# Performance work log

Measured on AMD Instinct MI355X. Metric: run time of the kernel, lower is better.

The kernel has to match this reference:

```python
import jax, jax.numpy as jnp
import numpy as np

D = 512      # model dim
NH = 8       # heads
DH = 64      # dim per head
M = 256      # num landmarks
ITERS = 6    # pinv iterations
EPS = 1e-5   # layernorm eps


def layer_norm(x, g, b):
    mu = x.mean(-1, keepdims=True)
    var = ((x - mu) ** 2).mean(-1, keepdims=True)
    return (x - mu) * jax.lax.rsqrt(var + EPS) * g + b


def moore_penrose_pinv(x, iters=ITERS):
    abs_x = jnp.abs(x)
    col = abs_x.sum(-1)
    row = abs_x.sum(-2)
    z = jnp.swapaxes(x, -1, -2) / (jnp.max(col) * jnp.max(row))
    I = jnp.eye(x.shape[-1], dtype=x.dtype)
    for _ in range(iters):
        xz = x @ z
        z = 0.25 * z @ (13 * I - xz @ (15 * I - xz @ (7 * I - xz)))
    return z


def nystrom_attention(x, w_qkv, w_out, b_out, res_w):
    B, n0, _ = x.shape
    pad = (M - n0 % M) % M
    x = jnp.pad(x, ((0, 0), (pad, 0), (0, 0)))  # pad at front, like lucidrains
    n = n0 + pad
    qkv = x @ w_qkv  # (B, n, 3*D), no bias
    q, k, v = jnp.split(qkv, 3, axis=-1)
    rs = lambda t: t.reshape(B, n, NH, DH).transpose(0, 2, 1, 3)  # (B,H,n,d)
    q = rs(q) * (DH ** -0.5)
    k = rs(k)
    v = rs(v)
    l = n // M
    q_l = q.reshape(B, NH, M, l, DH).mean(3)  # (B,H,M,d) landmark means
    k_l = k.reshape(B, NH, M, l, DH).mean(3)
    s1 = jnp.einsum('bhnd,bhmd->bhnm', q, k_l)
    s2 = jnp.einsum('bhmd,bhld->bhml', q_l, k_l)
    s3 = jnp.einsum('bhmd,bhnd->bhmn', q_l, k)
    a1 = jax.nn.softmax(s1, -1)
    a2 = jax.nn.softmax(s2, -1)
    a3 = jax.nn.softmax(s3, -1)
    out = a1 @ (moore_penrose_pinv(a2) @ (a3 @ v))  # (B,H,n,d)
    # depthwise residual conv over sequence: Conv2d(heads, heads, (33,1), groups=heads)
    res = jax.lax.conv_general_dilated(v, res_w, (1, 1), 'SAME',
                                       feature_group_count=NH,
                                       dimension_numbers=('NCHW', 'OIHW', 'NCHW'))
    out = out + res
    out = out.transpose(0, 2, 1, 3).reshape(B, n, NH * DH) @ w_out + b_out
    return out[:, -n0:]


def dwconv(x, w, b):
    y = jax.lax.conv_general_dilated(x, w, (1, 1), 'SAME',
                                     feature_group_count=x.shape[1],
                                     dimension_numbers=('NCHW', 'OIHW', 'NCHW'))
    return y + b[None, :, None, None]


def ppeg(x, pw7, pb7, pw5, pb5, pw3, pb3, Hh, Ww):
    cls, feat = x[:, :1], x[:, 1:]
    B, _, C = x.shape
    cnn = feat.transpose(0, 2, 1).reshape(B, C, Hh, Ww)
    y = cnn + dwconv(cnn, pw7, pb7) + dwconv(cnn, pw5, pb5) + dwconv(cnn, pw3, pb3)
    y = y.reshape(B, C, Hh * Ww).transpose(0, 2, 1)
    return jnp.concatenate([cls, y], axis=1)


def _forward(x, w_fc1, b_fc1, cls_token, ln1_g, ln1_b, qkv1_w, out1_w, out1_b, res1_w,
             ln2_g, ln2_b, qkv2_w, out2_w, out2_b, res2_w,
             pw7, pb7, pw5, pb5, pw3, pb3, lnf_g, lnf_b, w_fc2, b_fc2):
    h = jax.nn.relu(x @ w_fc1 + b_fc1)  # (B, N, 512)
    Hn = h.shape[1]
    s = int(np.ceil(np.sqrt(Hn)))  # static grid side
    add = s * s - Hn
    h = jnp.concatenate([h, h[:, :add]], axis=1)
    B = h.shape[0]
    cls = jnp.broadcast_to(cls_token, (B, 1, D))
    h = jnp.concatenate([cls, h], axis=1)
    h = h + nystrom_attention(layer_norm(h, ln1_g, ln1_b), qkv1_w, out1_w, out1_b, res1_w)
    h = ppeg(h, pw7, pb7, pw5, pb5, pw3, pb3, s, s)
    h = h + nystrom_attention(layer_norm(h, ln2_g, ln2_b), qkv2_w, out2_w, out2_b, res2_w)
    h = layer_norm(h, lnf_g, lnf_b)[:, 0]
    return h @ w_fc2 + b_fc2


def setup_inputs() -> dict:
    key = jax.random.key(0)
    ks = jax.random.split(key, 16)
    g = lambda k, shp, s=0.02: jax.random.normal(k, shp, dtype=jnp.float32) * s
    z = lambda n: jnp.zeros((n,), jnp.float32)
    o = lambda n: jnp.ones((n,), jnp.float32)
    B, N, DIN, NC = 2, 10000, 1024, 2
    return {
        'x': jax.random.normal(ks[0], (B, N, DIN), dtype=jnp.float32),
        'w_fc1': g(ks[1], (DIN, D)), 'b_fc1': z(D),
        'cls_token': g(ks[2], (1, 1, D), 1.0),
        'ln1_g': o(D), 'ln1_b': z(D),
        'qkv1_w': g(ks[3], (D, 3 * D)),
        'out1_w': g(ks[4], (D, D)), 'out1_b': z(D),
        'res1_w': g(ks[5], (NH, 1, 33, 1)),
        'ln2_g': o(D), 'ln2_b': z(D),
        'qkv2_w': g(ks[6], (D, 3 * D)),
        'out2_w': g(ks[7], (D, D)), 'out2_b': z(D),
        'res2_w': g(ks[8], (NH, 1, 33, 1)),
        'pw7': g(ks[9], (D, 1, 7, 7)), 'pb7': z(D),
        'pw5': g(ks[10], (D, 1, 5, 5)), 'pb5': z(D),
        'pw3': g(ks[11], (D, 1, 3, 3)), 'pb3': z(D),
        'lnf_g': o(D), 'lnf_b': z(D),
        'w_fc2': g(ks[12], (D, NC)), 'b_fc2': z(NC),
    }


def reference(x, w_fc1, b_fc1, cls_token, ln1_g, ln1_b, qkv1_w, out1_w, out1_b, res1_w,
              ln2_g, ln2_b, qkv2_w, out2_w, out2_b, res2_w,
              pw7, pb7, pw5, pb5, pw3, pb3, lnf_g, lnf_b, w_fc2, b_fc2):
    logits = _forward(x, w_fc1, b_fc1, cls_token, ln1_g, ln1_b, qkv1_w, out1_w, out1_b, res1_w,
                      ln2_g, ln2_b, qkv2_w, out2_w, out2_b, res2_w,
                      pw7, pb7, pw5, pb5, pw3, pb3, lnf_g, lnf_b, w_fc2, b_fc2)
    Y_prob = jax.nn.softmax(logits, -1)
    Y_hat = jnp.argmax(logits, -1)
    return logits, Y_prob, Y_hat
```

## Files before the change

kernel.cpp:

```cpp
#include <hip/hip_runtime.h>
#include <math.h>

#define FLAG_RELU 1
#define FLAG_BIAS 2
#define FLAG_ACC  4
#define FLAG_ATOMIC 8

static constexpr int BB   = 2;
static constexpr int N0   = 10000;
static constexpr int DIN  = 1024;
static constexpr int D    = 512;
static constexpr int NH   = 8;
static constexpr int DH   = 64;
static constexpr int MM   = 256;
static constexpr int SEQ  = 10240;
static constexpr int PADR = 239;
static constexpr int NTOK = 10001;
static constexpr int LL   = 40;
static constexpr float EPS_ = 1e-5f;

typedef short short8v __attribute__((ext_vector_type(8)));
typedef float f32x4 __attribute__((ext_vector_type(4)));

__device__ __forceinline__ void atomicMaxPosF(float* addr, float v) {
    atomicMax((unsigned int*)addr, __float_as_uint(v));
}
__device__ __forceinline__ ushort f2bf(float f) {
    unsigned u = __float_as_uint(f);
    return (ushort)((u + 0x7FFFu + ((u >> 16) & 1u)) >> 16);
}
__device__ __forceinline__ float bf2f(ushort h) {
    return __uint_as_float(((unsigned)h) << 16);
}
__device__ __forceinline__ void split4(float4 f, ushort* ph, ushort* pl) {
    ushort4 hv, lv;
    hv.x = f2bf(f.x); lv.x = f2bf(f.x - bf2f(hv.x));
    hv.y = f2bf(f.y); lv.y = f2bf(f.y - bf2f(hv.y));
    hv.z = f2bf(f.z); lv.z = f2bf(f.z - bf2f(hv.z));
    hv.w = f2bf(f.w); lv.w = f2bf(f.w - bf2f(hv.w));
    *(ushort4*)ph = hv; *(ushort4*)pl = lv;
}
__device__ __forceinline__ void split8r(const float* p, short8v& h, short8v& l) {
    ushort hb[8], lb[8];
    split4(*(const float4*)p,     &hb[0], &lb[0]);
    split4(*(const float4*)(p+4), &hb[4], &lb[4]);
    h = *(short8v*)hb; l = *(short8v*)lb;
}

__global__ __launch_bounds__(256)
void mgemm128(const float* __restrict__ A, int lda, long long sAz,
              const ushort* __restrict__ BtH, const ushort* __restrict__ BtL, int ldbt,
              float* __restrict__ C, int ldc, long long sCz, const float* __restrict__ bias,
              int M, int N, int K, int flags, int qcols, float qscale)
{
    __shared__ ushort AsH[4*128*8], AsL[4*128*8], BsH[4*128*8], BsL[4*128*8];
    A += (size_t)blockIdx.z * sAz;
    C += (size_t)blockIdx.z * sCz;
    int t = threadIdx.x;
    int m0 = blockIdx.y * 128, n0 = blockIdx.x * 128;
    int w = t >> 6, lane = t & 63, q = lane >> 4, r = lane & 15;
    int wm = w >> 1, wn = w & 1;
    f32x4 acc[4][4];
    #pragma unroll
    for (int i = 0; i < 4; i++)
        #pragma unroll
        for (int j = 0; j < 4; j++) acc[i][j] = (f32x4){0.f,0.f,0.f,0.f};

    int srow = t >> 1, scg = (t & 1) * 16;
    int qg = (t & 1) * 2;
    int gm = m0 + srow;
    float4 pa0, pa1, pa2, pa3;
    uint4  pb0, pb1, pb2, pb3;
    {
        pa0 = pa1 = pa2 = pa3 = make_float4(0,0,0,0);
        if (gm < M) {
            const float* ap = A + (size_t)gm * lda + scg;
            pa0 = *(const float4*)(ap);   pa1 = *(const float4*)(ap+4);
            pa2 = *(const float4*)(ap+8); pa3 = *(const float4*)(ap+12);
        }
        size_t gb = (size_t)(n0 + srow) * ldbt + scg;
        pb0 = *(const uint4*)(BtH + gb); pb1 = *(const uint4*)(BtH + gb + 8);
        pb2 = *(const uint4*)(BtL + gb); pb3 = *(const uint4*)(BtL + gb + 8);
    }
    for (int k0 = 0; k0 < K; k0 += 32) {
        {
            ushort hb[16], lb[16];
            split4(pa0, &hb[0],  &lb[0]);
            split4(pa1, &hb[4],  &lb[4]);
            split4(pa2, &hb[8],  &lb[8]);
            split4(pa3, &hb[12], &lb[12]);
            *(uint4*)&AsH[(qg  )*1024 + srow*8] = *(uint4*)&hb[0];
            *(uint4*)&AsH[(qg+1)*1024 + srow*8] = *(uint4*)&hb[8];
            *(uint4*)&AsL[(qg  )*1024 + srow*8] = *(uint4*)&lb[0];
            *(uint4*)&AsL[(qg+1)*1024 + srow*8] = *(uint4*)&lb[8];
            *(uint4*)&BsH[(qg  )*1024 + srow*8] = pb0;
            *(uint4*)&BsH[(qg+1)*1024 + srow*8] = pb1;
            *(uint4*)&BsL[(qg  )*1024 + srow*8] = pb2;
            *(uint4*)&BsL[(qg+1)*1024 + srow*8] = pb3;
        }
        __syncthreads();
        if (k0 + 32 < K) {
            pa0 = pa1 = pa2 = pa3 = make_float4(0,0,0,0);
            if (gm < M) {
                const float* ap = A + (size_t)gm * lda + k0 + 32 + scg;
                pa0 = *(const float4*)(ap);   pa1 = *(const float4*)(ap+4);
                pa2 = *(const float4*)(ap+8); pa3 = *(const float4*)(ap+12);
            }
            size_t gb = (size_t)(n0 + srow) * ldbt + k0 + 32 + scg;
            pb0 = *(const uint4*)(BtH + gb); pb1 = *(const uint4*)(BtH + gb + 8);
            pb2 = *(const uint4*)(BtL + gb); pb3 = *(const uint4*)(BtL + gb + 8);
        }
        short8v ah[4], al[4];
        #pragma unroll
        for (int mi = 0; mi < 4; mi++) {
            int row = wm*64 + mi*16 + r;
            ah[mi] = *(const short8v*)&AsH[q*1024 + row*8];
            al[mi] = *(const short8v*)&AsL[q*1024 + row*8];
        }
        #pragma unroll
        for (int ni = 0; ni < 4; ni++) {
            int col = wn*64 + ni*16 + r;
            short8v bh = *(const short8v*)&BsH[q*1024 + col*8];
            short8v bl = *(const short8v*)&BsL[q*1024 + col*8];
            #pragma unroll
            for (int mi = 0; mi < 4; mi++) {
                acc[mi][ni] = __builtin_amdgcn_mfma_f32_16x16x32_bf16(ah[mi], bh, acc[mi][ni], 0,0,0);
                acc[mi][ni] = __builtin_amdgcn_mfma_f32_16x16x32_bf16(ah[mi], bl, acc[mi][ni], 0,0,0);
                acc[mi][ni] = __builtin_amdgcn_mfma_f32_16x16x32_bf16(al[mi], bh, acc[mi][ni], 0,0,0);
            }
        }
        __syncthreads();
    }
    #pragma unroll
    for (int mi = 0; mi < 4; mi++)
        #pragma unroll
        for (int ni = 0; ni < 4; ni++) {
            int gcol = n0 + wn*64 + ni*16 + r;
            float qs = (gcol < qcols) ? qscale : 1.f;
            float bv = (flags & FLAG_BIAS) ? bias[gcol] : 0.f;
            #pragma unroll
            for (int rg = 0; rg < 4; rg++) {
                int grow = m0 + wm*64 + mi*16 + q*4 + rg;
                if (grow >= M) continue;
                float v = acc[mi][ni][rg] * qs + bv;
                if (flags & FLAG_RELU) v = fmaxf(v, 0.f);
                float* cp = C + (size_t)grow * ldc + gcol;
                if (flags & FLAG_ACC) v += *cp;
                *cp = v;
            }
        }
}

__global__ __launch_bounds__(256)
void mbgemm64(const float* __restrict__ Abase, long long sAb, long long sAh, long long sAz, int lda,
              const ushort* __restrict__ BtH, const ushort* __restrict__ BtL,
              const float* __restrict__ Bnt, long long sBb, long long sBh, int ldb,
              float* __restrict__ Cbase, long long sCb, long long sCh, long long sCz, int ldc,
              ushort* __restrict__ eTH, ushort* __restrict__ eTL, long long sT, int ldct,
              const float* __restrict__ rowM, const float* __restrict__ rowI,
              int M, int N, int K, int nchunk,
              float dg, float bsc, float osc, int slab0, int flags)
{
    __shared__ ushort AsH[4*64*8], AsL[4*64*8], BsH[4*64*8], BsL[4*64*8];
    int zi = blockIdx.z / nchunk, ch = blockIdx.z % nchunk;
    int g = slab0 + zi, b = g >> 3, h = g & 7;
    const float* A = Abase + (size_t)b*sAb + (size_t)h*sAh + (size_t)zi*sAz;
    float* C = Cbase ? (Cbase + (size_t)b*sCb + (size_t)h*sCh + (size_t)zi*sCz) : nullptr;
    int kpc = K / nchunk;
    int kb = ch * kpc, ke = kb + kpc;
    int t = threadIdx.x;
    int m0 = blockIdx.y * 64, n0 = blockIdx.x * 64;
    int w = t >> 6, lane = t & 63, q = lane >> 4, r = lane & 15;
    int wm = w >> 1, wn = w & 1;
    f32x4 acc[2][2];
    #pragma unroll
    for (int i = 0; i < 2; i++)
        #pragma unroll
        for (int j = 0; j < 2; j++) acc[i][j] = (f32x4){0.f,0.f,0.f,0.f};

    int srow = t >> 2, scg = (t & 3) * 8;
    int qg = t & 3;
    float rmv = 0.f, riv = 1.f;
    bool doexp = (rowM != nullptr);
    if (doexp) {
        rmv = rowM[(size_t)zi * MM + m0 + srow];
        riv = rowI[(size_t)zi * MM + m0 + srow];
    }
    const float* Abp = Bnt ? (Bnt + (size_t)b*sBb + (size_t)h*sBh) : nullptr;
    float4 pa0, pa1;
    float4 pf0, pf1;
    uint4  pu0, pu1;
    {
        const float* ap = A + (size_t)(m0 + srow) * lda + kb + scg;
        pa0 = *(const float4*)ap; pa1 = *(const float4*)(ap+4);
        if (Bnt) {
            const float* bp = Abp + (size_t)(n0 + srow) * ldb + kb + scg;
            pf0 = *(const float4*)bp; pf1 = *(const float4*)(bp+4);
        } else {
            size_t gb = (size_t)b*sBb + (size_t)h*sBh + (size_t)(n0 + srow) * ldb + kb + scg;
            pu0 = *(const uint4*)(BtH + gb); pu1 = *(const uint4*)(BtL + gb);
        }
    }
    for (int k0 = kb; k0 < ke; k0 += 32) {
        {
            float4 qa0 = pa0, qa1 = pa1;
            if (doexp) {
                qa0.x = expf(qa0.x - rmv) * riv; qa0.y = expf(qa0.y - rmv) * riv;
                qa0.z = expf(qa0.z - rmv) * riv; qa0.w = expf(qa0.w - rmv) * riv;
                qa1.x = expf(qa1.x - rmv) * riv; qa1.y = expf(qa1.y - rmv) * riv;
                qa1.z = expf(qa1.z - rmv) * riv; qa1.w = expf(qa1.w - rmv) * riv;
            }
            ushort hb[8], lb[8];
            split4(qa0, &hb[0], &lb[0]);
            split4(qa1, &hb[4], &lb[4]);
            *(uint4*)&AsH[qg*512 + srow*8] = *(uint4*)&hb[0];
            *(uint4*)&AsL[qg*512 + srow*8] = *(uint4*)&lb[0];
            if (Bnt) {
                ushort hc[8], lc[8];
                split4(pf0, &hc[0], &lc[0]);
                split4(pf1, &hc[4], &lc[4]);
                *(uint4*)&BsH[qg*512 + srow*8] = *(uint4*)&hc[0];
                *(uint4*)&BsL[qg*512 + srow*8] = *(uint4*)&lc[0];
            } else {
                *(uint4*)&BsH[qg*512 + srow*8] = pu0;
                *(uint4*)&BsL[qg*512 + srow*8] = pu1;
            }
        }
        __syncthreads();
        if (k0 + 32 < ke) {
            const float* ap = A + (size_t)(m0 + srow) * lda + k0 + 32 + scg;
            pa0 = *(const float4*)ap; pa1 = *(const float4*)(ap+4);
            if (Bnt) {
                const float* bp = Abp + (size_t)(n0 + srow) * ldb + k0 + 32 + scg;
                pf0 = *(const float4*)bp; pf1 = *(const float4*)(bp+4);
            } else {
                size_t gb = (size_t)b*sBb + (size_t)h*sBh + (size_t)(n0 + srow) * ldb + k0 + 32 + scg;
                pu0 = *(const uint4*)(BtH + gb); pu1 = *(const uint4*)(BtL + gb);
            }
        }
        short8v ah[2], al[2];
        #pragma unroll
        for (int mi = 0; mi < 2; mi++) {
            int row = wm*32 + mi*16 + r;
            ah[mi] = *(const short8v*)&AsH[q*512 + row*8];
            al[mi] = *(const short8v*)&AsL[q*512 + row*8];
        }
        #pragma unroll
        for (int ni = 0; ni < 2; ni++) {
            int col = wn*32 + ni*16 + r;
            short8v bh = *(const short8v*)&BsH[q*512 + col*8];
            short8v bl = *(const short8v*)&BsL[q*512 + col*8];
            #pragma unroll
            for (int mi = 0; mi < 2; mi++) {
                acc[mi][ni] = __builtin_amdgcn_mfma_f32_16x16x32_bf16(ah[mi], bh, acc[mi][ni], 0,0,0);
                acc[mi][ni] = __builtin_amdgcn_mfma_f32_16x16x32_bf16(ah[mi], bl, acc[mi][ni], 0,0,0);
                acc[mi][ni] = __builtin_amdgcn_mfma_f32_16x16x32_bf16(al[mi], bh, acc[mi][ni], 0,0,0);
            }
        }
        __syncthreads();
    }
    bool dgnz = (dg != 0.f);
    #pragma unroll
    for (int mi = 0; mi < 2; mi++)
        #pragma unroll
        for (int ni = 0; ni < 2; ni++) {
            int gm0 = m0 + wm*32 + mi*16 + q*4;
            int gn  = n0 + wn*32 + ni*16 + r;
            float v[4];
            #pragma unroll
            for (int rg = 0; rg < 4; rg++) {
                float u = bsc * acc[mi][ni][rg];
                if (dgnz) u += dg * A[(size_t)(gm0+rg) * lda + gn];
                v[rg] = osc * u;
            }
            if (C) {
                if (flags & FLAG_ATOMIC) {
                    #pragma unroll
                    for (int rg = 0; rg < 4; rg++)
                        atomicAdd(C + (size_t)(gm0+rg) * ldc + gn, v[rg]);
                } else {
                    #pragma unroll
                    for (int rg = 0; rg < 4; rg++)
                        C[(size_t)(gm0+rg) * ldc + gn] = v[rg];
                }
            }
            if (eTH) {
                ushort4 hv, lv;
                hv.x = f2bf(v[0]); lv.x = f2bf(v[0] - bf2f(hv.x));
                hv.y = f2bf(v[1]); lv.y = f2bf(v[1] - bf2f(hv.y));
                hv.z = f2bf(v[2]); lv.z = f2bf(v[2] - bf2f(hv.z));
                hv.w = f2bf(v[3]); lv.w = f2bf(v[3] - bf2f(hv.w));
                size_t to = (size_t)g * sT + (size_t)gn * ldct + gm0;
                *(ushort4*)(eTH + to) = hv;
                *(ushort4*)(eTL + to) = lv;
            }
        }
}

__global__ __launch_bounds__(256)
void a1_fused(const float* __restrict__ qkv,
              const ushort* __restrict__ klH, const ushort* __restrict__ klL,
              const ushort* __restrict__ wbH, const ushort* __restrict__ wbL,
              float* __restrict__ attn)
{
    constexpr int LP = 264;
    __shared__ ushort PcH[32*LP], PcL[32*LP];
    __shared__ float redm[4][32];
    __shared__ float reds[4][32];
    int g = blockIdx.y, b = g >> 3, h = g & 7;
    int tok0 = blockIdx.x * 32;
    int t = threadIdx.x;
    int w = t >> 6, lane = t & 63, q = lane >> 4, r = lane & 15;

    f32x4 acc[2][4];
    #pragma unroll
    for (int i = 0; i < 2; i++)
        #pragma unroll
        for (int j = 0; j < 4; j++) acc[i][j] = (f32x4){0.f,0.f,0.f,0.f};
    #pragma unroll
    for (int k0 = 0; k0 < 64; k0 += 32) {
        short8v ah[2], al[2];
        #pragma unroll
        for (int mi = 0; mi < 2; mi++) {
            const float* ap = qkv + ((size_t)b*SEQ + tok0 + mi*16 + r) * 1536
                            + h*DH + k0 + q*8;
            split8r(ap, ah[mi], al[mi]);
        }
        #pragma unroll
        for (int ni = 0; ni < 4; ni++) {
            size_t kb = ((size_t)g*MM + w*64 + ni*16 + r) * DH + k0 + q*8;
            short8v bh = *(const short8v*)(klH + kb);
            short8v bl = *(const short8v*)(klL + kb);
            #pragma unroll
            for (int mi = 0; mi < 2; mi++) {
                acc[mi][ni] = __builtin_amdgcn_mfma_f32_16x16x32_bf16(ah[mi], bh, acc[mi][ni], 0,0,0);
                acc[mi][ni] = __builtin_amdgcn_mfma_f32_16x16x32_bf16(ah[mi], bl, acc[mi][ni], 0,0,0);
                acc[mi][ni] = __builtin_amdgcn_mfma_f32_16x16x32_bf16(al[mi], bh, acc[mi][ni], 0,0,0);
            }
        }
    }
    #pragma unroll
    for (int mi = 0; mi < 2; mi++)
        #pragma unroll
        for (int rg = 0; rg < 4; rg++) {
            float m = fmaxf(fmaxf(acc[mi][0][rg], acc[mi][1][rg]),
                            fmaxf(acc[mi][2][rg], acc[mi][3][rg]));
            for (int o = 8; o > 0; o >>= 1) m = fmaxf(m, __shfl_xor(m, o));
            if (r == 0) redm[w][mi*16 + q*4 + rg] = m;
        }
    __syncthreads();
    #pragma unroll
    for (int mi = 0; mi < 2; mi++)
        #pragma unroll
        for (int rg = 0; rg < 4; rg++) {
            int row = mi*16 + q*4 + rg;
            float gm = fmaxf(fmaxf(redm[0][row], redm[1][row]),
                             fmaxf(redm[2][row], redm[3][row]));
            float s = 0.f;
            #pragma unroll
            for (int ni = 0; ni < 4; ni++) {
                float e = expf(acc[mi][ni][rg] - gm);
                acc[mi][ni][rg] = e;
                s += e;
                int col = w*64 + ni*16 + r;
                ushort hv = f2bf(e);
                PcH[row*LP + col] = hv;
                PcL[row*LP + col] = f2bf(e - bf2f(hv));
            }
            for (int o = 8; o > 0; o >>= 1) s += __shfl_xor(s, o);
            if (r == 0) reds[w][row] = s;
        }
    __syncthreads();
    int wm = w & 1, wn = w >> 1;
    int prow = wm*16 + r;
    f32x4 oacc[2];
    #pragma unroll
    for (int ni = 0; ni < 2; ni++) oacc[ni] = (f32x4){0.f,0.f,0.f,0.f};
    #pragma unroll
    for (int k0 = 0; k0 < 8; k0++) {
        short8v ph = *(const short8v*)&PcH[prow*LP + k0*32 + q*8];
        short8v pl = *(const short8v*)&PcL[prow*LP + k0*32 + q*8];
        #pragma unroll
        for (int ni = 0; ni < 2; ni++) {
            size_t wo = ((size_t)g*64 + wn*32 + ni*16 + r) * MM + k0*32 + q*8;
            short8v bh = *(const short8v*)(wbH + wo);
            short8v bl = *(const short8v*)(wbL + wo);
            oacc[ni] = __builtin_amdgcn_mfma_f32_16x16x32_bf16(ph, bh, oacc[ni], 0,0,0);
            oacc[ni] = __builtin_amdgcn_mfma_f32_16x16x32_bf16(ph, bl, oacc[ni], 0,0,0);
            oacc[ni] = __builtin_amdgcn_mfma_f32_16x16x32_bf16(pl, bh, oacc[ni], 0,0,0);
        }
    }
    float inv[4];
    #pragma unroll
    for (int rg = 0; rg < 4; rg++) {
        int row = wm*16 + q*4 + rg;
        inv[rg] = 1.0f / (reds[0][row] + reds[1][row] + reds[2][row] + reds[3][row]);
    }
    #pragma unroll
    for (int ni = 0; ni < 2; ni++)
        #pragma unroll
        for (int rg = 0; rg < 4; rg++) {
            int tok = tok0 + wm*16 + q*4 + rg;
            attn[((size_t)b*SEQ + tok) * D + h*DH + wn*32 + ni*16 + r] = oacc[ni][rg] * inv[rg];
        }
}

__global__ __launch_bounds__(256)
void convsplitT(const float* __restrict__ in, ushort* __restrict__ oh, ushort* __restrict__ ol,
                int R, int C, int ldin, long long sInB, long long sInH, long long sInZ,
                int ldo, long long sOutZ)
{
    __shared__ float tile[32][33];
    int z = blockIdx.z, b = z >> 3, h = z & 7;
    const float* I = in + (size_t)b*sInB + (size_t)h*sInH + (size_t)z*sInZ;
    int p0 = blockIdx.x * 32, c0 = blockIdx.y * 32;
    int tx = threadIdx.x & 31, ty = threadIdx.x >> 5;
    #pragma unroll
    for (int k = 0; k < 4; k++) {
        int rr = p0 + ty + k*8, cc = c0 + tx;
        tile[ty + k*8][tx] = (rr < R && cc < C) ? I[(size_t)rr * ldin + cc] : 0.f;
    }
    __syncthreads();
    #pragma unroll
    for (int k = 0; k < 4; k++) {
        int rr = p0 + tx, cc = c0 + ty + k*8;
        if (rr < R && cc < C) {
            float f = tile[tx][ty + k*8];
            ushort hv = f2bf(f);
            size_t o = (size_t)z * sOutZ + (size_t)cc * ldo + rr;
            oh[o] = hv; ol[o] = f2bf(f - bf2f(hv));
        }
    }
}

__global__ void fill_cls(const float* __restrict__ cls, float* __restrict__ H) {
    H[(size_t)blockIdx.x * NTOK * D + threadIdx.x] = cls[threadIdx.x];
}

__global__ __launch_bounds__(256)
void ln_pad(const float* __restrict__ H, const float* __restrict__ g,
            const float* __restrict__ bt, float* __restrict__ out)
{
    int blk = blockIdx.x;
    int b = blk / SEQ, i = blk % SEQ;
    int t = threadIdx.x;
    float* orow = out + (size_t)blk * D;
    if (i < PADR) { orow[t] = 0.f; orow[t+256] = 0.f; return; }
    const float* x = H + ((size_t)b * NTOK + (i - PADR)) * D;
    float v0 = x[t], v1 = x[t+256];
    __shared__ float w1[4], w2[4];
    float s = v0 + v1;
    for (int o = 32; o > 0; o >>= 1) s += __shfl_xor(s, o);
    if ((t & 63) == 0) w1[t >> 6] = s;
    __syncthreads();
    float mu = (w1[0]+w1[1]+w1[2]+w1[3]) * (1.0f / D);
    float d0 = v0 - mu, d1 = v1 - mu;
    float qq = d0*d0 + d1*d1;
    for (int o = 32; o > 0; o >>= 1) qq += __shfl_xor(qq, o);
    if ((t & 63) == 0) w2[t >> 6] = qq;
    __syncthreads();
    float rs = rsqrtf((w2[0]+w2[1]+w2[2]+w2[3]) * (1.0f / D) + EPS_);
    orow[t]     = d0 * rs * g[t]     + bt[t];
    orow[t+256] = d1 * rs * g[t+256] + bt[t+256];
}

__global__ __launch_bounds__(512)
void landmarks(const float* __restrict__ qkv, float* __restrict__ ql,
               float* __restrict__ klt, ushort* __restrict__ klH, ushort* __restrict__ klL)
{
    int blk = blockIdx.x;
    int b = blk >> 8, m = blk & 255;
    int c = threadIdx.x;
    const float* base = qkv + ((size_t)b * SEQ + (size_t)m * LL) * 1536;
    float sq0=0,sq1=0,sq2=0,sq3=0, sk0=0,sk1=0,sk2=0,sk3=0;
    for (int tt = 0; tt < LL; tt += 4) {
        const float* rr = base + (size_t)tt * 1536;
        sq0 += rr[c];          sk0 += rr[512 + c];
        sq1 += rr[1536 + c];   sk1 += rr[1536 + 512 + c];
        sq2 += rr[3072 + c];   sk2 += rr[3072 + 512 + c];
        sq3 += rr[4608 + c];   sk3 += rr[4608 + 512 + c];
    }
    float sq = (sq0+sq1+sq2+sq3) * (1.0f / LL);
    float sk = (sk0+sk1+sk2+sk3) * (1.0f / LL);
    int h = c >> 6, d = c & 63;
    int slab = b * NH + h;
    ql [((size_t)slab * MM + m) * DH + d] = sq;
    klt[((size_t)slab * DH + d) * MM + m] = sk;
    size_t kidx = ((size_t)slab * MM + m) * DH + d;
    ushort kh = f2bf(sk);
    klH[kidx] = kh; klL[kidx] = f2bf(sk - bf2f(kh));
}

__global__ __launch_bounds__(256)
void s2_softmax(const float* __restrict__ ql, const float* __restrict__ klt,
                float* __restrict__ a2)
{
    int blk = blockIdx.x;
    int m = blk & 255, slab = blk >> 8;
    int j = threadIdx.x;
    __shared__ float q[64];
    __shared__ float red[256];
    if (j < 64) q[j] = ql[((size_t)slab * MM + m) * DH + j];
    __syncthreads();
    const float* kt = klt + (size_t)slab * DH * MM;
    float s = 0.f;
    #pragma unroll 8
    for (int kk = 0; kk < 64; kk++) s = fmaf(q[kk], kt[kk*MM + j], s);
    red[j] = s; __syncthreads();
    for (int o = 128; o > 0; o >>= 1) { if (j < o) red[j] = fmaxf(red[j], red[j+o]); __syncthreads(); }
    float mx = red[0]; __syncthreads();
    float e = expf(s - mx);
    red[j] = e; __syncthreads();
    for (int o = 128; o > 0; o >>= 1) { if (j < o) red[j] += red[j+o]; __syncthreads(); }
    a2[((size_t)slab * MM + m) * MM + j] = e / red[0];
}

__global__ void zero_scr(float* s) { if (threadIdx.x < 2) s[threadIdx.x] = 0.f; }

__global__ __launch_bounds__(256)
void a2_alpha(const float* __restrict__ a2, float* __restrict__ scr)
{
    int slab = blockIdx.x, t = threadIdx.x;
    const float* A = a2 + (size_t)slab * MM * MM;
    float cs = 0.f, rs = 0.f;
    for (int rr = 0; rr < MM; rr++) cs += fabsf(A[(size_t)rr * MM + t]);
    for (int cc = 0; cc < MM; cc++) rs += fabsf(A[(size_t)t * MM + cc]);
    __shared__ float red[256];
    red[t] = rs; __syncthreads();
    for (int o = 128; o > 0; o >>= 1) { if (t < o) red[t] = fmaxf(red[t], red[t+o]); __syncthreads(); }
    float mrs = red[0]; __syncthreads();
    red[t] = cs; __syncthreads();
    for (int o = 128; o > 0; o >>= 1) { if (t < o) red[t] = fmaxf(red[t], red[t+o]); __syncthreads(); }
    float mcs = red[0];
    if (t == 0) { atomicMaxPosF(scr + 0, mrs); atomicMaxPosF(scr + 1, mcs); }
}

__global__ __launch_bounds__(256)
void z_init(const float* __restrict__ a2, const float* __restrict__ scr,
            float* __restrict__ z, ushort* __restrict__ zTh, ushort* __restrict__ zTl)
{
    size_t idx = (size_t)blockIdx.x * 256 + threadIdx.x;
    int slab = (int)(idx >> 16), rr = (int)((idx >> 8) & 255), cc = (int)(idx & 255);
    float inv = 1.0f / (scr[0] * scr[1]);
    z[idx] = a2[((size_t)slab << 16) + (size_t)cc * MM + rr] * inv;
    float tv = a2[idx] * inv;
    ushort th = f2bf(tv);
    zTh[idx] = th; zTl[idx] = f2bf(tv - bf2f(th));
}

__global__ __launch_bounds__(256)
void s3_maxsum(const float* __restrict__ s3, float* __restrict__ rowM,
               float* __restrict__ rowI)
{
    const float* row = s3 + (size_t)blockIdx.x * SEQ;
    int t = threadIdx.x;
    float4 v[10];
    #pragma unroll
    for (int i = 0; i < 10; i++) v[i] = *(const float4*)(row + 4*(i*256 + t));
    float mx = -3.4e38f;
    #pragma unroll
    for (int i = 0; i < 10; i++)
        mx = fmaxf(mx, fmaxf(fmaxf(v[i].x, v[i].y), fmaxf(v[i].z, v[i].w)));
    __shared__ float red[4];
    for (int o = 32; o > 0; o >>= 1) mx = fmaxf(mx, __shfl_xor(mx, o));
    if ((t & 63) == 0) red[t >> 6] = mx;
    __syncthreads();
    mx = fmaxf(fmaxf(red[0], red[1]), fmaxf(red[2], red[3]));
    float sum = 0.f;
    #pragma unroll
    for (int i = 0; i < 10; i++) {
        sum += expf(v[i].x - mx) + expf(v[i].y - mx)
             + expf(v[i].z - mx) + expf(v[i].w - mx);
    }
    __shared__ float red2[4];
    for (int o = 32; o > 0; o >>= 1) sum += __shfl_xor(sum, o);
    if ((t & 63) == 0) red2[t >> 6] = sum;
    __syncthreads();
    if (t == 0) {
        rowM[blockIdx.x] = mx;
        rowI[blockIdx.x] = 1.0f / (red2[0] + red2[1] + red2[2] + red2[3]);
    }
}

__global__ __launch_bounds__(512)
void res_add(const float* __restrict__ qkv, const float* __restrict__ rw,
             float* __restrict__ attn)
{
    int blk = blockIdx.x;
    int b = blk / (SEQ/16), i0 = (blk % (SEQ/16)) * 16;
    int c = threadIdx.x, h = c >> 6;
    __shared__ float w[NH*33];
    if (c < NH*33) w[c] = rw[c];
    __syncthreads();
    float acc[16];
    float* ab = attn + ((size_t)b * SEQ + i0) * D + c;
    #pragma unroll
    for (int rr = 0; rr < 16; rr++) acc[rr] = ab[(size_t)rr * D];
    const float* vb = qkv + (size_t)b * SEQ * 1536 + 2*D + c;
    const float* wh = w + h * 33;
    #pragma unroll 4
    for (int jj = 0; jj < 48; jj++) {
        int j = i0 + jj - 16;
        float val = ((unsigned)j < (unsigned)SEQ) ? vb[(size_t)j * 1536] : 0.f;
        #pragma unroll
        for (int rr = 0; rr < 16; rr++) {
            int ky = jj - rr;
            if (ky >= 0 && ky < 33) acc[rr] = fmaf(val, wh[ky], acc[rr]);
        }
    }
    #pragma unroll
    for (int rr = 0; rr < 16; rr++) ab[(size_t)rr * D] = acc[rr];
}

__global__ __launch_bounds__(256)
void t_fw(const float* __restrict__ H, float* __restrict__ P)
{
    __shared__ float tile[32][33];
    int p0 = blockIdx.x * 32, c0 = blockIdx.y * 32, b = blockIdx.z;
    int tx = threadIdx.x & 31, ty = threadIdx.x >> 5;
    #pragma unroll
    for (int k = 0; k < 4; k++) {
        int pos = p0 + ty + k*8;
        tile[ty + k*8][tx] = (pos < 10000)
            ? H[((size_t)b * NTOK + 1 + pos) * D + c0 + tx] : 0.f;
    }
    __syncthreads();
    #pragma unroll
    for (int k = 0; k < 4; k++) {
        int c = c0 + ty + k*8, pos = p0 + tx;
        if (pos < 10000)
            P[((size_t)b * D + c) * 10000 + pos] = tile[tx][ty + k*8];
    }
}

__global__ __launch_bounds__(256)
void ppeg_conv(const float* __restrict__ P,
               const float* __restrict__ w7, const float* __restrict__ b7,
               const float* __restrict__ w5, const float* __restrict__ b5,
               const float* __restrict__ w3, const float* __restrict__ b3,
               float* __restrict__ Q)
{
    __shared__ float PS[106 * 107];
    __shared__ float w7s[49], w5s[25], w3s[9];
    int blk = blockIdx.x;
    int b = blk >> 9, c = blk & 511;
    int t = threadIdx.x;
    for (int idx = t; idx < 106*107; idx += 256) PS[idx] = 0.f;
    if (t < 49) w7s[t] = w7[(size_t)c * 49 + t];
    if (t < 25) w5s[t] = w5[(size_t)c * 25 + t];
    if (t < 9)  w3s[t] = w3[(size_t)c * 9 + t];
    float bsum = b7[c] + b5[c] + b3[c];
    __syncthreads();
    const float* Pin = P + ((size_t)b * D + c) * 10000;
    for (int p = t; p < 10000; p += 256) {
        int y = p / 100, x = p - y * 100;
        PS[(y + 3) * 107 + x + 3] = Pin[p];
    }
    __syncthreads();
    float* Qo = Q + ((size_t)b * D + c) * 10000;
    for (int task = t; task < 2500; task += 256) {
        int ry = task / 100, x = task - ry * 100;
        int y0 = ry * 4;
        float a0 = bsum + PS[(y0+3)*107 + x+3];
        float a1 = bsum + PS[(y0+4)*107 + x+3];
        float a2 = bsum + PS[(y0+5)*107 + x+3];
        float a3 = bsum + PS[(y0+6)*107 + x+3];
        #pragma unroll
        for (int rr = 0; rr < 10; rr++) {
            const float* rp = &PS[(y0 + rr) * 107 + x];
            #pragma unroll
            for (int kx = 0; kx < 7; kx++) {
                float v = rp[kx];
                if (rr < 7)            a0 = fmaf(v, w7s[rr*7 + kx], a0);
                if (rr >= 1 && rr < 8) a1 = fmaf(v, w7s[(rr-1)*7 + kx], a1);
                if (rr >= 2 && rr < 9) a2 = fmaf(v, w7s[(rr-2)*7 + kx], a2);
                if (rr >= 3)           a3 = fmaf(v, w7s[(rr-3)*7 + kx], a3);
            }
        }
        #pragma unroll
        for (int rr = 0; rr < 8; rr++) {
            const float* rp = &PS[(y0 + rr + 1) * 107 + x + 1];
            #pragma unroll
            for (int kx = 0; kx < 5; kx++) {
                float v = rp[kx];
                if (rr < 5)            a0 = fmaf(v, w5s[rr*5 + kx], a0);
                if (rr >= 1 && rr < 6) a1 = fmaf(v, w5s[(rr-1)*5 + kx], a1);
                if (rr >= 2 && rr < 7) a2 = fmaf(v, w5s[(rr-2)*5 + kx], a2);
                if (rr >= 3)           a3 = fmaf(v, w5s[(rr-3)*5 + kx], a3);
            }
        }
        #pragma unroll
        for (int rr = 0; rr < 6; rr++) {
            const float* rp = &PS[(y0 + rr + 2) * 107 + x + 2];
            #pragma unroll
            for (int kx = 0; kx < 3; kx++) {
                float v = rp[kx];
                if (rr < 3)            a0 = fmaf(v, w3s[rr*3 + kx], a0);
                if (rr >= 1 && rr < 4) a1 = fmaf(v, w3s[(rr-1)*3 + kx], a1);
                if (rr >= 2 && rr < 5) a2 = fmaf(v, w3s[(rr-2)*3 + kx], a2);
                if (rr >= 3)           a3 = fmaf(v, w3s[(rr-3)*3 + kx], a3);
            }
        }
        Qo[(y0+0)*100 + x] = a0;
        Qo[(y0+1)*100 + x] = a1;
        Qo[(y0+2)*100 + x] = a2;
        Qo[(y0+3)*100 + x] = a3;
    }
}

__global__ __launch_bounds__(256)
void t_bw(const float* __restrict__ Q, float* __restrict__ H)
{
    __shared__ float tile[32][33];
    int p0 = blockIdx.x * 32, c0 = blockIdx.y * 32, b = blockIdx.z;
    int tx = threadIdx.x & 31, ty = threadIdx.x >> 5;
    #pragma unroll
    for (int k = 0; k < 4; k++) {
        int c = c0 + ty + k*8, pos = p0 + tx;
        tile[ty + k*8][tx] = (pos < 10000)
            ? Q[((size_t)b * D + c) * 10000 + pos] : 0.f;
    }
    __syncthreads();
    #pragma unroll
    for (int k = 0; k < 4; k++) {
        int pos = p0 + ty + k*8;
        if (pos < 10000)
            H[((size_t)b * NTOK + 1 + pos) * D + c0 + tx] = tile[tx][ty + k*8];
    }
}

__global__ __launch_bounds__(512)
void final_head(const float* __restrict__ H, const float* __restrict__ g,
                const float* __restrict__ bt, const float* __restrict__ w2,
                const float* __restrict__ b2, float* __restrict__ out)
{
    int b = blockIdx.x, t = threadIdx.x;
    __shared__ float red[512];
    float v = H[(size_t)b * NTOK * D + t];
    red[t] = v; __syncthreads();
    for (int o = 256; o > 0; o >>= 1) { if (t < o) red[t] += red[t+o]; __syncthreads(); }
    float mu = red[0] * (1.0f / D); __syncthreads();
    float dv = v - mu;
    red[t] = dv*dv; __syncthreads();
    for (int o = 256; o > 0; o >>= 1) { if (t < o) red[t] += red[t+o]; __syncthreads(); }
    float rstd = rsqrtf(red[0] * (1.0f / D) + EPS_); __syncthreads();
    float xn = dv * rstd * g[t] + bt[t];
    red[t] = xn * w2[2*t]; __syncthreads();
    for (int o = 256; o > 0; o >>= 1) { if (t < o) red[t] += red[t+o]; __syncthreads(); }
    float l0 = red[0] + b2[0]; __syncthreads();
    red[t] = xn * w2[2*t+1]; __syncthreads();
    for (int o = 256; o > 0; o >>= 1) { if (t < o) red[t] += red[t+o]; __syncthreads(); }
    float l1 = red[0] + b2[1];
    if (t == 0) {
        out[b*2+0] = l0; out[b*2+1] = l1;
        float mx = fmaxf(l0, l1);
        float e0 = expf(l0 - mx), e1 = expf(l1 - mx);
        float ssum = e0 + e1;
        out[4 + b*2 + 0] = e0 / ssum;
        out[4 + b*2 + 1] = e1 / ssum;
        out[8 + b] = (l1 > l0) ? 1.0f : 0.0f;
    }
}

extern "C" void kernel_launch(void* const* d_in, const int* in_sizes, int n_in,
                              void* d_out, int out_size, void* d_ws, size_t ws_size,
                              hipStream_t stream)
{
    const float* x      = (const float*)d_in[0];
    const float* w_fc1  = (const float*)d_in[1];
    const float* b_fc1  = (const float*)d_in[2];
    const float* cls    = (const float*)d_in[3];
    const float* ln1_g  = (const float*)d_in[4];
    const float* ln1_b  = (const float*)d_in[5];
    const float* qkv1_w = (const float*)d_in[6];
    const float* out1_w = (const float*)d_in[7];
    const float* out1_b = (const float*)d_in[8];
    const float* res1_w = (const float*)d_in[9];
    const float* ln2_g  = (const float*)d_in[10];
    const float* ln2_b  = (const float*)d_in[11];
    const float* qkv2_w = (const float*)d_in[12];
    const float* out2_w = (const float*)d_in[13];
    const float* out2_b = (const float*)d_in[14];
    const float* res2_w = (const float*)d_in[15];
    const float* pw7 = (const float*)d_in[16];
    const float* pb7 = (const float*)d_in[17];
    const float* pw5 = (const float*)d_in[18];
    const float* pb5 = (const float*)d_in[19];
    const float* pw3 = (const float*)d_in[20];
    const float* pb3 = (const float*)d_in[21];
    const float* lnf_g = (const float*)d_in[22];
    const float* lnf_b = (const float*)d_in[23];
    const float* w_fc2 = (const float*)d_in[24];
    const float* b_fc2 = (const float*)d_in[25];

    float* ws = (float*)d_ws;
    size_t off = 0;
    auto alloc = [&](size_t n) { float* p = ws + off; off += (n + 63) & ~(size_t)63; return p; };
    float* H    = alloc((size_t)BB * NTOK * D);
    float* LN   = alloc((size_t)BB * SEQ * D);
    float* QKV  = alloc((size_t)BB * SEQ * 3 * D);
    float* QL   = alloc((size_t)BB * NH * MM * DH);
    float* KLT  = alloc((size_t)BB * NH * DH * MM);
    float* A2   = alloc((size_t)BB * NH * MM * MM);
    float* ZA   = alloc((size_t)BB * NH * MM * MM);
    float* ZB   = alloc((size_t)BB * NH * MM * MM);
    float* XZ   = alloc((size_t)BB * NH * MM * MM);
    float* A3V  = alloc((size_t)BB * NH * MM * DH);
    float* WB   = alloc((size_t)BB * NH * MM * DH);
    float* S3   = alloc((size_t)8 * MM * SEQ);
    float* SCR  = alloc(64);
    float* ROWM = alloc((size_t)8 * MM);
    float* ROWI = alloc((size_t)8 * MM);
    auto ualloc = [&](size_t n) { ushort* p = (ushort*)(ws + off); off += ((n + 127) / 2) & ~(size_t)63; return p; };
    ushort* WTfcH = ualloc((size_t)512 * 1024);
    ushort* WTfcL = ualloc((size_t)512 * 1024);
    ushort* WTqH  = ualloc((size_t)1536 * 512);
    ushort* WTqL  = ualloc((size_t)1536 * 512);
    ushort* WToH  = ualloc((size_t)512 * 512);
    ushort* WToL  = ualloc((size_t)512 * 512);
    ushort* klBH  = ualloc((size_t)16 * MM * DH);
    ushort* klBL  = ualloc((size_t)16 * MM * DH);
    float*  ATTN = LN;
    ushort* VTH  = (ushort*)LN;
    ushort* VTL  = VTH + (size_t)16 * DH * SEQ;
    ushort* A3VTH = (ushort*)ZB;
    ushort* A3VTL = A3VTH + (size_t)16 * DH * MM;
    ushort* WBTH  = A3VTL + (size_t)16 * DH * MM;
    ushort* WBTL  = WBTH  + (size_t)16 * DH * MM;
    ushort* PT   = (ushort*)S3;
    const size_t PS_ = (size_t)16 * 65536;
    ushort* zTAH = PT;            ushort* zTAL = PT + PS_;
    ushort* zTBH = PT + 2*PS_;    ushort* zTBL = PT + 3*PS_;
    ushort* XZTH = PT + 4*PS_;    ushort* XZTL = PT + 5*PS_;
    ushort* T1TH = PT + 6*PS_;    ushort* T1TL = PT + 7*PS_;
    ushort* T2TH = PT + 8*PS_;    ushort* T2TL = PT + 9*PS_;
    (void)ws_size; (void)in_sizes; (void)n_in; (void)out_size;

    convsplitT<<<dim3(32,16,1), 256, 0, stream>>>(w_fc1, WTfcH, WTfcL, 1024, 512, 512, 0,0,0, 1024, 0);
    mgemm128<<<dim3(4, 79, BB), 256, 0, stream>>>(x, DIN, (long long)N0*DIN,
        WTfcH, WTfcL, 1024, H + D, D, (long long)NTOK*D, b_fc1,
        N0, D, DIN, FLAG_BIAS|FLAG_RELU, 0, 1.f);
    fill_cls<<<BB, D, 0, stream>>>(cls, H);

    auto attention = [&](const float* lg, const float* lb,
                         const float* qw, const float* ow,
                         const float* ob, const float* rw)
    {
        convsplitT<<<dim3(16,48,1), 256, 0, stream>>>(qw, WTqH, WTqL, 512, 1536, 1536, 0,0,0, 512, 0);
        convsplitT<<<dim3(16,16,1), 256, 0, stream>>>(ow, WToH, WToL, 512, 512, 512, 0,0,0, 512, 0);
        ln_pad<<<BB*SEQ, 256, 0, stream>>>(H, lg, lb, LN);
        mgemm128<<<dim3(12, 160, 1), 256, 0, stream>>>(LN, D, 0, WTqH, WTqL, D,
            QKV, 3*D, 0, nullptr, BB*SEQ, 3*D, D, 0, D, 0.125f);
        convsplitT<<<dim3(320, 2, 16), 256, 0, stream>>>(QKV + 2*D, VTH, VTL,
            SEQ, DH, 1536, (long long)SEQ*1536, 64, 0, SEQ, (long long)DH*SEQ);
        landmarks<<<BB*MM, 512, 0, stream>>>(QKV, QL, KLT, klBH, klBL);
        s2_softmax<<<BB*NH*MM, 256, 0, stream>>>(QL, KLT, A2);
        zero_scr<<<1, 64, 0, stream>>>(SCR);
        a2_alpha<<<BB*NH, 256, 0, stream>>>(A2, SCR);
        z_init<<<BB*NH*MM*MM/256, 256, 0, stream>>>(A2, SCR, ZA, zTAH, zTAL);
        float* z = ZA; float* zn = ZB;
        ushort *zTcH = zTAH, *zTcL = zTAL, *zTnH = zTBH, *zTnL = zTBL;
        for (int it = 0; it < 6; it++) {
            dim3 g(4, 4, 16);
            mbgemm64<<<g,256,0,stream>>>(A2, 0,0,65536LL, MM,
                zTcH, zTcL, nullptr, 8LL*65536, 65536LL, MM,
                XZ, 0,0,65536LL, MM, XZTH, XZTL, 65536LL, MM,
                nullptr, nullptr,
                MM, MM, MM, 1, 0.f, 1.f, 1.f, 0, 0);
            mbgemm64<<<g,256,0,stream>>>(XZ, 0,0,65536LL, MM,
                XZTH, XZTL, nullptr, 8LL*65536, 65536LL, MM,
                nullptr, 0,0,0, MM, T1TH, T1TL, 65536LL, MM,
                nullptr, nullptr,
                MM, MM, MM, 1, 7.f, -1.f, 1.f, 0, 0);
            mbgemm64<<<g,256,0,stream>>>(XZ, 0,0,65536LL, MM,
                T1TH, T1TL, nullptr, 8LL*65536, 65536LL, MM,
                nullptr, 0,0,0, MM, T2TH, T2TL, 65536LL, MM,
                nullptr, nullptr,
                MM, MM, MM, 1, 15.f, -1.f, 1.f, 0, 0);
            mbgemm64<<<g,256,0,stream>>>(z, 0,0,65536LL, MM,
                T2TH, T2TL, nullptr, 8LL*65536, 65536LL, MM,
                zn, 0,0,65536LL, MM, zTnH, zTnL, 65536LL, MM,
                nullptr, nullptr,
                MM, MM, MM, 1, 13.f, -1.f, 0.25f, 0, 0);
            float* ts = z; z = zn; zn = ts;
            ushort* uh = zTcH; zTcH = zTnH; zTnH = uh;
            ushort* ul = zTcL; zTcL = zTnL; zTnL = ul;
        }
        for (int grp = 0; grp < 2; grp++) {
            int slab0 = grp * 8;
            mbgemm64<<<dim3(160, 4, 8), 256, 0, stream>>>(QL, 8LL*16384, 16384LL, 0, DH,
                nullptr, nullptr, QKV + D, (long long)SEQ*1536, 64LL, 1536,
                S3, 0,0,(long long)MM*SEQ, SEQ, nullptr, nullptr, 0, 0,
                nullptr, nullptr,
                MM, SEQ, DH, 1, 0.f, 1.f, 1.f, slab0, 0);
            s3_maxsum<<<8*MM, 256, 0, stream>>>(S3, ROWM, ROWI);
            hipMemsetAsync(A3V + (size_t)slab0 * MM * DH, 0,
                           (size_t)8 * MM * DH * sizeof(float), stream);
            mbgemm64<<<dim3(1, 4, 8*16), 256, 0, stream>>>(S3, 0,0,(long long)MM*SEQ, SEQ,
                VTH, VTL, nullptr, 8LL*DH*SEQ, (long long)DH*SEQ, SEQ,
                A3V, 8LL*16384, 16384LL, 0, DH, nullptr, nullptr, 0, 0,
                ROWM, ROWI,
                MM, DH, SEQ, 16, 0.f, 1.f, 1.f, slab0, FLAG_ATOMIC);
        }
        convsplitT<<<dim3(8, 2, 16), 256, 0, stream>>>(A3V, A3VTH, A3VTL,
            MM, DH, DH, 0, 0, 16384LL, MM, 16384LL);
        mbgemm64<<<dim3(1, 4, 16), 256, 0, stream>>>(z, 0,0,65536LL, MM,
            A3VTH, A3VTL, nullptr, 8LL*16384, 16384LL, MM,
            WB, 8LL*16384, 16384LL, 0, DH, WBTH, WBTL, 16384LL, MM,
            nullptr, nullptr,
            MM, DH, MM, 1, 0.f, 1.f, 1.f, 0, 0);
        a1_fused<<<dim3(SEQ/32, 16), 256, 0, stream>>>(QKV, klBH, klBL, WBTH, WBTL, ATTN);
        res_add<<<BB*SEQ/16, 512, 0, stream>>>(QKV, rw, ATTN);
        mgemm128<<<dim3(4, 79, BB), 256, 0, stream>>>(ATTN + (size_t)PADR*D, D, (long long)SEQ*D,
            WToH, WToL, D, H, D, (long long)NTOK*D, ob,
            NTOK, D, D, FLAG_BIAS|FLAG_ACC, 0, 1.f);
    };

    attention(ln1_g, ln1_b, qkv1_w, out1_w, out1_b, res1_w);

    {
        float* Pp = S3;
        float* Qp = S3 + (size_t)BB * D * 10000;
        dim3 tg((10000 + 31)/32, D/32, BB);
        t_fw<<<tg, 256, 0, stream>>>(H, Pp);
        ppeg_conv<<<BB*D, 256, 0, stream>>>(Pp, pw7, pb7, pw5, pb5, pw3, pb3, Qp);
        t_bw<<<tg, 256, 0, stream>>>(Qp, H);
    }

    attention(ln2_g, ln2_b, qkv2_w, out2_w, out2_b, res2_w);

    final_head<<<BB, 512, 0, stream>>>(H, lnf_g, lnf_b, w_fc2, b_fc2, (float*)d_out);
}
```

Before: 2.371 ms.

## Use fast exp intrinsics and prefetch MFMA operands in fused attention kernel

Replaces expf with __expf in several softmax paths (GEMM A-operand exp, a1_fused, s2 softmax, s3 row stats) to cut transcendental instruction cost. In a1_fused, hoists the landmark-key loads ahead of the MFMA loop and double-buffers the weight operand loads so global memory latency overlaps with MFMA work. It also adds a min-blocks-per-CU hint of 4 to raise occupancy, at the risk of register pressure or spills and slightly lower exp accuracy.

Measured after the change: 2.342 ms. About the same (-1.2%).

```diff
diff --git a/kernel.cpp b/kernel.cpp
--- a/kernel.cpp
+++ b/kernel.cpp
@@ -205,10 +205,10 @@
         {
             float4 qa0 = pa0, qa1 = pa1;
             if (doexp) {
-                qa0.x = expf(qa0.x - rmv) * riv; qa0.y = expf(qa0.y - rmv) * riv;
-                qa0.z = expf(qa0.z - rmv) * riv; qa0.w = expf(qa0.w - rmv) * riv;
-                qa1.x = expf(qa1.x - rmv) * riv; qa1.y = expf(qa1.y - rmv) * riv;
-                qa1.z = expf(qa1.z - rmv) * riv; qa1.w = expf(qa1.w - rmv) * riv;
+                qa0.x = __expf(qa0.x - rmv) * riv; qa0.y = __expf(qa0.y - rmv) * riv;
+                qa0.z = __expf(qa0.z - rmv) * riv; qa0.w = __expf(qa0.w - rmv) * riv;
+                qa1.x = __expf(qa1.x - rmv) * riv; qa1.y = __expf(qa1.y - rmv) * riv;
+                qa1.z = __expf(qa1.z - rmv) * riv; qa1.w = __expf(qa1.w - rmv) * riv;
             }
             ushort hb[8], lb[8];
             split4(qa0, &hb[0], &lb[0]);
@@ -297,7 +297,7 @@
         }
 }
 
-__global__ __launch_bounds__(256)
+__global__ __launch_bounds__(256, 4)
 void a1_fused(const float* __restrict__ qkv,
               const ushort* __restrict__ klH, const ushort* __restrict__ klL,
               const ushort* __restrict__ wbH, const ushort* __restrict__ wbL,
@@ -319,6 +319,13 @@
         for (int j = 0; j < 4; j++) acc[i][j] = (f32x4){0.f,0.f,0.f,0.f};
     #pragma unroll
     for (int k0 = 0; k0 < 64; k0 += 32) {
+        short8v bh[4], bl[4];
+        #pragma unroll
+        for (int ni = 0; ni < 4; ni++) {
+            size_t kb = ((size_t)g*MM + w*64 + ni*16 + r) * DH + k0 + q*8;
+            bh[ni] = *(const short8v*)(klH + kb);
+            bl[ni] = *(const short8v*)(klL + kb);
+        }
         short8v ah[2], al[2];
         #pragma unroll
         for (int mi = 0; mi < 2; mi++) {
@@ -328,14 +335,11 @@
         }
         #pragma unroll
         for (int ni = 0; ni < 4; ni++) {
-            size_t kb = ((size_t)g*MM + w*64 + ni*16 + r) * DH + k0 + q*8;
-            short8v bh = *(const short8v*)(klH + kb);
-            short8v bl = *(const short8v*)(klL + kb);
             #pragma unroll
             for (int mi = 0; mi < 2; mi++) {
-                acc[mi][ni] = __builtin_amdgcn_mfma_f32_16x16x32_bf16(ah[mi], bh, acc[mi][ni], 0,0,0);
-                acc[mi][ni] = __builtin_amdgcn_mfma_f32_16x16x32_bf16(ah[mi], bl, acc[mi][ni], 0,0,0);
-                acc[mi][ni] = __builtin_amdgcn_mfma_f32_16x16x32_bf16(al[mi], bh, acc[mi][ni], 0,0,0);
+                acc[mi][ni] = __builtin_amdgcn_mfma_f32_16x16x32_bf16(ah[mi], bh[ni], acc[mi][ni], 0,0,0);
+                acc[mi][ni] = __builtin_amdgcn_mfma_f32_16x16x32_bf16(ah[mi], bl[ni], acc[mi][ni], 0,0,0);
+                acc[mi][ni] = __builtin_amdgcn_mfma_f32_16x16x32_bf16(al[mi], bh[ni], acc[mi][ni], 0,0,0);
             }
         }
     }
@@ -359,7 +363,7 @@
             float s = 0.f;
             #pragma unroll
             for (int ni = 0; ni < 4; ni++) {
-                float e = expf(acc[mi][ni][rg] - gm);
+                float e = __expf(acc[mi][ni][rg] - gm);
                 acc[mi][ni][rg] = e;
                 s += e;
                 int col = w*64 + ni*16 + r;
@@ -376,15 +380,34 @@
     f32x4 oacc[2];
     #pragma unroll
     for (int ni = 0; ni < 2; ni++) oacc[ni] = (f32x4){0.f,0.f,0.f,0.f};
+    short8v wh0[2], wl0[2], wh1[2], wl1[2];
+    #pragma unroll
+    for (int ni = 0; ni < 2; ni++) {
+        size_t wo = ((size_t)g*64 + wn*32 + ni*16 + r) * MM + q*8;
+        wh0[ni] = *(const short8v*)(wbH + wo);
+        wl0[ni] = *(const short8v*)(wbL + wo);
+    }
     #pragma unroll
     for (int k0 = 0; k0 < 8; k0++) {
         short8v ph = *(const short8v*)&PcH[prow*LP + k0*32 + q*8];
         short8v pl = *(const short8v*)&PcL[prow*LP + k0*32 + q*8];
+        if (k0 < 7) {
+            #pragma unroll
+            for (int ni = 0; ni < 2; ni++) {
+                size_t wo = ((size_t)g*64 + wn*32 + ni*16 + r) * MM + (k0+1)*32 + q*8;
+                if (k0 & 1) {
+                    wh0[ni] = *(const short8v*)(wbH + wo);
+                    wl0[ni] = *(const short8v*)(wbL + wo);
+                } else {
+                    wh1[ni] = *(const short8v*)(wbH + wo);
+                    wl1[ni] = *(const short8v*)(wbL + wo);
+                }
+            }
+        }
         #pragma unroll
         for (int ni = 0; ni < 2; ni++) {
-            size_t wo = ((size_t)g*64 + wn*32 + ni*16 + r) * MM + k0*32 + q*8;
-            short8v bh = *(const short8v*)(wbH + wo);
-            short8v bl = *(const short8v*)(wbL + wo);
+            short8v bh = (k0 & 1) ? wh1[ni] : wh0[ni];
+            short8v bl = (k0 & 1) ? wl1[ni] : wl0[ni];
             oacc[ni] = __builtin_amdgcn_mfma_f32_16x16x32_bf16(ph, bh, oacc[ni], 0,0,0);
             oacc[ni] = __builtin_amdgcn_mfma_f32_16x16x32_bf16(ph, bl, oacc[ni], 0,0,0);
             oacc[ni] = __builtin_amdgcn_mfma_f32_16x16x32_bf16(pl, bh, oacc[ni], 0,0,0);
@@ -509,7 +532,7 @@
     red[j] = s; __syncthreads();
     for (int o = 128; o > 0; o >>= 1) { if (j < o) red[j] = fmaxf(red[j], red[j+o]); __syncthreads(); }
     float mx = red[0]; __syncthreads();
-    float e = expf(s - mx);
+    float e = __expf(s - mx);
     red[j] = e; __syncthreads();
     for (int o = 128; o > 0; o >>= 1) { if (j < o) red[j] += red[j+o]; __syncthreads(); }
     a2[((size_t)slab * MM + m) * MM + j] = e / red[0];
@@ -569,8 +592,8 @@
     float sum = 0.f;
     #pragma unroll
     for (int i = 0; i < 10; i++) {
-        sum += expf(v[i].x - mx) + expf(v[i].y - mx)
-             + expf(v[i].z - mx) + expf(v[i].w - mx);
+        sum += __expf(v[i].x - mx) + __expf(v[i].y - mx)
+             + __expf(v[i].z - mx) + __expf(v[i].w - mx);
     }
     __shared__ float red2[4];
     for (int o = 32; o > 0; o >>= 1) sum += __shfl_xor(sum, o);
```
